# Optimization experiments

Hardware: AMD Instinct MI355X
Metric: run time of the kernel (lower is better)

The kernel has to match this reference:

```python
import jax, jax.numpy as jnp
import numpy as np

BITS = 8
MAX_DELTA = 2.5
QMAX = 2 ** (BITS - 1) - 1  # 127
EPS = 1e-5
K = 3  # kernel size


def _quantize(w):
    # symmetric uniform quantization to `BITS` bits, clamped at +/- MAX_DELTA
    scale = MAX_DELTA / QMAX
    return jnp.clip(jnp.round(w / scale), -QMAX, QMAX) * scale


def _adder_conv(x, wq):
    # AdderNet 'convolution': out[n,co,h,w] = -sum_{ci,kh,kw} |x_patch - wq|
    # x: [N, Cin, H, W]; wq: [Cout, Cin, K, K]; stride 1, padding 1 (same size)
    N, Cin, H, W = x.shape
    Cout = wq.shape[0]
    xp = jnp.pad(x, ((0, 0), (0, 0), (1, 1), (1, 1)))
    out = jnp.zeros((N, Cout, H, W), x.dtype)
    for kh in range(K):            # fixed small loop over kernel taps
        for kw in range(K):
            xs = xp[:, :, kh:kh + H, kw:kw + W]      # [N,Cin,H,W]
            wk = wq[:, :, kh, kw]                    # [Cout,Cin]
            # broadcast [N,1,Cin,H,W] - [1,Cout,Cin,1,1], reduce Cin
            out = out - jnp.sum(jnp.abs(xs[:, None] - wk[None, :, :, None, None]), axis=2)
    return out


def _bn_adder(x, gamma, beta, wb):
    # BatchNorm2d (training-mode batch stats) with the adder weight-bias
    # (per-channel mean |quantized weight|) synced into the affine bias.
    mu = jnp.mean(x, axis=(0, 2, 3), keepdims=True)
    var = jnp.var(x, axis=(0, 2, 3), keepdims=True)
    c = lambda v: v.reshape(1, -1, 1, 1)
    return c(gamma) * (x - mu) * jax.lax.rsqrt(var + EPS) + c(beta) + c(wb)


def setup_inputs() -> dict:
    key = jax.random.key(0)
    k = jax.random.split(key, 3)
    N, C, H, W = 32, 32, 32, 32
    x = jax.random.normal(k[0], (N, C, H, W), jnp.float32)
    w1 = jax.random.normal(k[1], (C, C, K, K), jnp.float32) * 0.1
    w2 = jax.random.normal(k[2], (C, C, K, K), jnp.float32) * 0.1
    return {
        "x": x,
        "w1": w1, "gamma1": jnp.ones(C, jnp.float32), "beta1": jnp.zeros(C, jnp.float32),
        "w2": w2, "gamma2": jnp.ones(C, jnp.float32), "beta2": jnp.zeros(C, jnp.float32),
    }


def reference(x, w1, gamma1, beta1, w2, gamma2, beta2):
    residual = x
    wq1 = _quantize(w1)
    out = _adder_conv(x, wq1)
    wb1 = jnp.mean(jnp.abs(wq1), axis=(1, 2, 3))   # adder weight bias, per out-channel
    out = _bn_adder(out, gamma1, beta1, wb1)
    out = jax.nn.relu(out)
    wq2 = _quantize(w2)
    out = _adder_conv(out, wq2)
    wb2 = jnp.mean(jnp.abs(wq2), axis=(1, 2, 3))
    out = _bn_adder(out, gamma2, beta2, wb2)
    out = jax.nn.relu(out + residual)
    return out
```

## Files before the change

kernel.cpp:

```cpp
#include <hip/hip_runtime.h>


#define QSCALE (2.5f / 127.f)

__device__ __forceinline__ float quantf(float w) {
  float v = rintf(w * (1.0f / QSCALE));
  v = fminf(fmaxf(v, -127.f), 127.f);
  return v * QSCALE;
}

__global__ __launch_bounds__(256) void quant_k(const float* __restrict__ w1,
                                               const float* __restrict__ w2,
                                               float* __restrict__ q1,
                                               float* __restrict__ q2) {
  int i = blockIdx.x * 256 + threadIdx.x;
  if (i >= 18432) return;
  const float* w = (i < 9216) ? w1 : w2;
  float* dst = (i < 9216) ? q1 : q2;
  int j = (i < 9216) ? i : i - 9216;
  int co = j / 288;
  int r = j - co * 288;
  dst[r * 32 + co] = quantf(w[j]);
}

template <bool AFFINE>
__global__ __launch_bounds__(1024, 4) void conv_k(
    const float* __restrict__ in,
    const float* __restrict__ wq,
    const float* __restrict__ ps_prev,
    const float* __restrict__ pq_prev,
    const float* __restrict__ wq_prev,
    const float* __restrict__ gprev,
    const float* __restrict__ bprev,
    float* __restrict__ outb,
    float* __restrict__ ps_out,
    float* __restrict__ pq_out) {
  __shared__ __align__(16) float smem[16128];
  __shared__ float r2a[32][32], r2b[32][32], r2c[32][32];
  __shared__ float abuf[32], bbuf[32];

  float* xs = smem;
  float* wls = smem + 6912;

  const int tid = threadIdx.x;
  const int blk = blockIdx.x;
  const int n = blk >> 3, rg = blk & 7;
  const int h0 = rg << 2;

  if (AFFINE) {
    const int c = tid & 31, ch = tid >> 5;
    float s = 0.f, q = 0.f;
    #pragma unroll
    for (int k = 0; k < 8; ++k) {
      s += ps_prev[(ch * 8 + k) * 32 + c];
      q += pq_prev[(ch * 8 + k) * 32 + c];
    }
    float wbp = 0.f;
    #pragma unroll
    for (int uu = 0; uu < 9; ++uu)
      wbp += fabsf(wq_prev[(ch * 9 + uu) * 32 + c]);
    r2a[c][ch] = s; r2b[c][ch] = q; r2c[c][ch] = wbp;
    __syncthreads();
    if (tid < 32) {
      double S = 0.0, Q = 0.0; float W = 0.f;
      #pragma unroll 8
      for (int k = 0; k < 32; ++k) {
        S += (double)r2a[tid][k]; Q += (double)r2b[tid][k]; W += r2c[tid][k];
      }
      const double M = 32768.0;
      const double mu = S / M;
      const double var = Q / M - mu * mu;
      const double inv = 1.0 / sqrt(var + 1e-5);
      const double g = (double)gprev[tid];
      abuf[tid] = (float)(g * inv);
      bbuf[tid] = (float)((double)bprev[tid] + (double)(W * (1.f / 288.f)) - g * inv * mu);
    }
    __syncthreads();
  }

  {
    const float4* src = (const float4*)wq;
    float4* dst = (float4*)wls;
    for (int i = tid; i < 2304; i += 1024) dst[i] = src[i];
  }
  for (int i = tid; i < 1728; i += 1024) {
    const int ci = i / 54;
    const int rem = i - ci * 54;
    const int tr = rem / 9, k = rem - tr * 9;
    const int h = h0 - 1 + tr;
    float* dst = xs + ci * 216 + tr * 36;
    if (k < 8) {
      float4 v = {0.f, 0.f, 0.f, 0.f};
      if ((unsigned)h < 32u) {
        v = *(const float4*)(in + (((n * 32 + ci) * 32 + h) * 32 + 4 * k));
        if (AFFINE) {
          const float av = abuf[ci], bv = bbuf[ci];
          v.x = fmaxf(fmaf(av, v.x, bv), 0.f);
          v.y = fmaxf(fmaf(av, v.y, bv), 0.f);
          v.z = fmaxf(fmaf(av, v.z, bv), 0.f);
          v.w = fmaxf(fmaf(av, v.w, bv), 0.f);
        }
      }
      dst[4 * k + 1] = v.x; dst[4 * k + 2] = v.y;
      dst[4 * k + 3] = v.z; dst[4 * k + 4] = v.w;
    } else {
      dst[0] = 0.f; dst[33] = 0.f; dst[34] = 0.f; dst[35] = 0.f;
    }
  }
  __syncthreads();

  const int wv = tid >> 6;
  const int oct = wv & 3, slice = wv >> 2;
  const int l = tid & 63;
  const int quad = l >> 5, p = l & 31;
  const int row = p >> 3, g = p & 7;

  float acc[4][4];
  #pragma unroll
  for (int j = 0; j < 4; ++j)
    #pragma unroll
    for (int k = 0; k < 4; ++k) acc[j][k] = 0.f;

  const float* xpb = xs + row * 36 + 4 * g;
  const float* wpb = wls + oct * 8 + quad * 4;

  #pragma unroll 2
  for (int cc = 0; cc < 8; ++cc) {
    const int ci = slice * 8 + cc;
    const float* xp = xpb + ci * 216;
    float xw[3][6];
    #pragma unroll
    for (int kh = 0; kh < 3; ++kh) {
      const float4 A = *(const float4*)(xp + kh * 36);
      const float2 B = *(const float2*)(xp + kh * 36 + 4);
      xw[kh][0] = A.x; xw[kh][1] = A.y; xw[kh][2] = A.z; xw[kh][3] = A.w;
      xw[kh][4] = B.x; xw[kh][5] = B.y;
    }
    const float* wp = wpb + ci * 288;
    #pragma unroll
    for (int t = 0; t < 9; ++t) {
      const float4 W = *(const float4*)(wp + t * 32);
      const int kh = t / 3, kw = t - kh * 3;
      #pragma unroll
      for (int j = 0; j < 4; ++j) {
        const float xv = xw[kh][j + kw];
        acc[j][0] += fabsf(xv - W.x);
        acc[j][1] += fabsf(xv - W.y);
        acc[j][2] += fabsf(xv - W.z);
        acc[j][3] += fabsf(xv - W.w);
      }
    }
  }
  __syncthreads();

  float* red = smem;
  const int lane16 = oct * 64 + l;
  if (slice != 0) {
    const int sb = (slice - 1) * 16;
    #pragma unroll
    for (int j = 0; j < 4; ++j)
      #pragma unroll
      for (int k = 0; k < 4; ++k)
        red[(sb + j * 4 + k) * 256 + lane16] = acc[j][k];
  }
  __syncthreads();

  if (slice == 0) {
    #pragma unroll
    for (int s = 0; s < 3; ++s)
      #pragma unroll
      for (int j = 0; j < 4; ++j)
        #pragma unroll
        for (int k = 0; k < 4; ++k)
          acc[j][k] += red[(s * 16 + j * 4 + k) * 256 + lane16];

    const int h = h0 + row;
    float sv[4], qv[4];
    #pragma unroll
    for (int k = 0; k < 4; ++k) {
      const int co = oct * 8 + quad * 4 + k;
      float4 st;
      st.x = -acc[0][k]; st.y = -acc[1][k]; st.z = -acc[2][k]; st.w = -acc[3][k];
      *(float4*)&outb[((n * 32 + co) * 32 + h) * 32 + 4 * g] = st;
      sv[k] = st.x + st.y + st.z + st.w;
      qv[k] = st.x*st.x + st.y*st.y + st.z*st.z + st.w*st.w;
    }
    #pragma unroll
    for (int d = 1; d < 32; d <<= 1) {
      #pragma unroll
      for (int k = 0; k < 4; ++k) {
        sv[k] += __shfl_xor(sv[k], d);
        qv[k] += __shfl_xor(qv[k], d);
      }
    }
    if (p == 0) {
      const int chunk = n * 8 + rg;
      float4 s4; s4.x = sv[0]; s4.y = sv[1]; s4.z = sv[2]; s4.w = sv[3];
      float4 q4; q4.x = qv[0]; q4.y = qv[1]; q4.z = qv[2]; q4.w = qv[3];
      ((float4*)(ps_out + chunk * 32))[oct * 2 + quad] = s4;
      ((float4*)(pq_out + chunk * 32))[oct * 2 + quad] = q4;
    }
  }
}

__global__ __launch_bounds__(512) void final_k(
    const float* __restrict__ o2, const float* __restrict__ xres,
    const float* __restrict__ ps, const float* __restrict__ pq,
    const float* __restrict__ wq2, const float* __restrict__ g2,
    const float* __restrict__ b2, float* __restrict__ out) {
  __shared__ float r2a[32][16], r2b[32][16], r2c[32][16];
  __shared__ float abuf[32], bbuf[32];
  const int tid = threadIdx.x;
  const int c = tid & 31, ch = tid >> 5;
  float s = 0.f, q = 0.f;
  #pragma unroll
  for (int k = 0; k < 16; ++k) {
    s += ps[(ch * 16 + k) * 32 + c];
    q += pq[(ch * 16 + k) * 32 + c];
  }
  float wbp = 0.f;
  #pragma unroll
  for (int uu = 0; uu < 18; ++uu)
    wbp += fabsf(wq2[(ch * 18 + uu) * 32 + c]);
  r2a[c][ch] = s; r2b[c][ch] = q; r2c[c][ch] = wbp;
  __syncthreads();
  if (tid < 32) {
    double S = 0.0, Q = 0.0; float W = 0.f;
    #pragma unroll
    for (int k = 0; k < 16; ++k) {
      S += (double)r2a[tid][k]; Q += (double)r2b[tid][k]; W += r2c[tid][k];
    }
    const double M = 32768.0;
    const double mu = S / M;
    const double var = Q / M - mu * mu;
    const double inv = 1.0 / sqrt(var + 1e-5);
    const double g = (double)g2[tid];
    abuf[tid] = (float)(g * inv);
    bbuf[tid] = (float)((double)b2[tid] + (double)(W * (1.f / 288.f)) - g * inv * mu);
  }
  __syncthreads();

  const int f4 = blockIdx.x * 512 + tid;
  const int cc = (f4 >> 8) & 31;
  const float4 o = ((const float4*)o2)[f4];
  const float4 xr = ((const float4*)xres)[f4];
  const float av = abuf[cc], bvv = bbuf[cc];
  float4 r;
  r.x = fmaxf(fmaf(av, o.x, bvv) + xr.x, 0.f);
  r.y = fmaxf(fmaf(av, o.y, bvv) + xr.y, 0.f);
  r.z = fmaxf(fmaf(av, o.z, bvv) + xr.z, 0.f);
  r.w = fmaxf(fmaf(av, o.w, bvv) + xr.w, 0.f);
  ((float4*)out)[f4] = r;
}

extern "C" void kernel_launch(void* const* d_in, const int* in_sizes, int n_in,
                              void* d_out, int out_size, void* d_ws, size_t ws_size,
                              hipStream_t stream) {
  const float* x   = (const float*)d_in[0];
  const float* w1  = (const float*)d_in[1];
  const float* g1  = (const float*)d_in[2];
  const float* be1 = (const float*)d_in[3];
  const float* w2  = (const float*)d_in[4];
  const float* g2  = (const float*)d_in[5];
  const float* be2 = (const float*)d_in[6];
  float* ws = (float*)d_ws;

  float* WQ1 = ws;
  float* WQ2 = ws + 9216;
  float* PS1 = ws + 18432;
  float* PQ1 = ws + 26624;
  float* PS2 = ws + 34816;
  float* PQ2 = ws + 43008;
  float* O1  = ws + 51200;
  float* O2  = O1 + 1048576;
  float* out = (float*)d_out;

  quant_k<<<72, 256, 0, stream>>>(w1, w2, WQ1, WQ2);
  conv_k<false><<<256, 1024, 0, stream>>>(x, WQ1, nullptr, nullptr, nullptr,
                                          nullptr, nullptr, O1, PS1, PQ1);
  conv_k<true><<<256, 1024, 0, stream>>>(O1, WQ2, PS1, PQ1, WQ1, g1, be1,
                                         O2, PS2, PQ2);
  final_k<<<512, 512, 0, stream>>>(O2, x, PS2, PQ2, WQ2, g2, be2, out);
}
```

Before: 60.06 us.

## Split conv input channels across two blocks and add merge kernel for stats

Each conv kernel now processes half of the input channels per block, doubling the grid to 512 blocks and cutting shared memory per block. Partial outputs go to separate buffers, and a new merge kernel sums the halves and computes per-sample, per-channel sum and sum-of-squares for batch norm. The intent is more parallelism and occupancy in the conv stage. In exchange it adds two kernel launches and extra global memory round trips for the partial outputs.

```diff
diff --git a/kernel.cpp b/kernel.cpp
--- a/kernel.cpp
+++ b/kernel.cpp
@@ -32,40 +32,40 @@
     const float* __restrict__ wq_prev,
     const float* __restrict__ gprev,
     const float* __restrict__ bprev,
-    float* __restrict__ outb,
-    float* __restrict__ ps_out,
-    float* __restrict__ pq_out) {
-  __shared__ __align__(16) float smem[16128];
-  __shared__ float r2a[32][32], r2b[32][32], r2c[32][32];
+    float* __restrict__ outb) {
+  __shared__ __align__(16) float smem[12288];
   __shared__ float abuf[32], bbuf[32];
 
   float* xs = smem;
-  float* wls = smem + 6912;
+  float* wls = smem + 3456;
 
   const int tid = threadIdx.x;
   const int blk = blockIdx.x;
-  const int n = blk >> 3, rg = blk & 7;
+  const int n = blk >> 4;
+  const int rg = (blk >> 1) & 7;
+  const int cih = blk & 1;
   const int h0 = rg << 2;
 
   if (AFFINE) {
+    float* r2a = smem;
+    float* r2b = smem + 1024;
+    float* r2c = smem + 2048;
     const int c = tid & 31, ch = tid >> 5;
-    float s = 0.f, q = 0.f;
-    #pragma unroll
-    for (int k = 0; k < 8; ++k) {
-      s += ps_prev[(ch * 8 + k) * 32 + c];
-      q += pq_prev[(ch * 8 + k) * 32 + c];
-    }
+    const float s = ps_prev[ch * 32 + c];
+    const float q = pq_prev[ch * 32 + c];
     float wbp = 0.f;
     #pragma unroll
     for (int uu = 0; uu < 9; ++uu)
       wbp += fabsf(wq_prev[(ch * 9 + uu) * 32 + c]);
-    r2a[c][ch] = s; r2b[c][ch] = q; r2c[c][ch] = wbp;
+    r2a[c * 32 + ch] = s; r2b[c * 32 + ch] = q; r2c[c * 32 + ch] = wbp;
     __syncthreads();
     if (tid < 32) {
       double S = 0.0, Q = 0.0; float W = 0.f;
       #pragma unroll 8
       for (int k = 0; k < 32; ++k) {
-        S += (double)r2a[tid][k]; Q += (double)r2b[tid][k]; W += r2c[tid][k];
+        S += (double)r2a[tid * 32 + k];
+        Q += (double)r2b[tid * 32 + k];
+        W += r2c[tid * 32 + k];
       }
       const double M = 32768.0;
       const double mu = S / M;
@@ -81,14 +81,15 @@
   {
     const float4* src = (const float4*)wq;
     float4* dst = (float4*)wls;
-    for (int i = tid; i < 2304; i += 1024) dst[i] = src[i];
-  }
-  for (int i = tid; i < 1728; i += 1024) {
-    const int ci = i / 54;
-    const int rem = i - ci * 54;
+    for (int i = tid; i < 1152; i += 1024) dst[i] = src[cih * 1152 + i];
+  }
+  if (tid < 864) {
+    const int lci = tid / 54;
+    const int rem = tid - lci * 54;
     const int tr = rem / 9, k = rem - tr * 9;
+    const int ci = cih * 16 + lci;
     const int h = h0 - 1 + tr;
-    float* dst = xs + ci * 216 + tr * 36;
+    float* dst = xs + lci * 216 + tr * 36;
     if (k < 8) {
       float4 v = {0.f, 0.f, 0.f, 0.f};
       if ((unsigned)h < 32u) {
@@ -123,11 +124,12 @@
 
   const float* xpb = xs + row * 36 + 4 * g;
   const float* wpb = wls + oct * 8 + quad * 4;
+  const int lci0 = slice * 4;
 
   #pragma unroll 2
-  for (int cc = 0; cc < 8; ++cc) {
-    const int ci = slice * 8 + cc;
-    const float* xp = xpb + ci * 216;
+  for (int cc = 0; cc < 4; ++cc) {
+    const int lci = lci0 + cc;
+    const float* xp = xpb + lci * 216;
     float xw[3][6];
     #pragma unroll
     for (int kh = 0; kh < 3; ++kh) {
@@ -136,7 +138,7 @@
       xw[kh][0] = A.x; xw[kh][1] = A.y; xw[kh][2] = A.z; xw[kh][3] = A.w;
       xw[kh][4] = B.x; xw[kh][5] = B.y;
     }
-    const float* wp = wpb + ci * 288;
+    const float* wp = wpb + lci * 288;
     #pragma unroll
     for (int t = 0; t < 9; ++t) {
       const float4 W = *(const float4*)(wp + t * 32);
@@ -174,32 +176,44 @@
         for (int k = 0; k < 4; ++k)
           acc[j][k] += red[(s * 16 + j * 4 + k) * 256 + lane16];
 
+    float* OUT = outb + cih * 1048576;
     const int h = h0 + row;
-    float sv[4], qv[4];
     #pragma unroll
     for (int k = 0; k < 4; ++k) {
       const int co = oct * 8 + quad * 4 + k;
       float4 st;
       st.x = -acc[0][k]; st.y = -acc[1][k]; st.z = -acc[2][k]; st.w = -acc[3][k];
-      *(float4*)&outb[((n * 32 + co) * 32 + h) * 32 + 4 * g] = st;
-      sv[k] = st.x + st.y + st.z + st.w;
-      qv[k] = st.x*st.x + st.y*st.y + st.z*st.z + st.w*st.w;
-    }
-    #pragma unroll
-    for (int d = 1; d < 32; d <<= 1) {
-      #pragma unroll
-      for (int k = 0; k < 4; ++k) {
-        sv[k] += __shfl_xor(sv[k], d);
-        qv[k] += __shfl_xor(qv[k], d);
-      }
-    }
-    if (p == 0) {
-      const int chunk = n * 8 + rg;
-      float4 s4; s4.x = sv[0]; s4.y = sv[1]; s4.z = sv[2]; s4.w = sv[3];
-      float4 q4; q4.x = qv[0]; q4.y = qv[1]; q4.z = qv[2]; q4.w = qv[3];
-      ((float4*)(ps_out + chunk * 32))[oct * 2 + quad] = s4;
-      ((float4*)(pq_out + chunk * 32))[oct * 2 + quad] = q4;
-    }
+      *(float4*)&OUT[((n * 32 + co) * 32 + h) * 32 + 4 * g] = st;
+    }
+  }
+}
+
+__global__ __launch_bounds__(512) void merge_k(
+    float* __restrict__ A, const float* __restrict__ B,
+    float* __restrict__ ps, float* __restrict__ pq) {
+  __shared__ float pss[8], pqq[8];
+  const int tid = threadIdx.x;
+  const int b = blockIdx.x;
+  const int f4 = b * 512 + tid;
+  const float4 a = ((const float4*)A)[f4];
+  const float4 bb = ((const float4*)B)[f4];
+  float4 v;
+  v.x = a.x + bb.x; v.y = a.y + bb.y; v.z = a.z + bb.z; v.w = a.w + bb.w;
+  ((float4*)A)[f4] = v;
+  float s = v.x + v.y + v.z + v.w;
+  float q = v.x*v.x + v.y*v.y + v.z*v.z + v.w*v.w;
+  #pragma unroll
+  for (int d = 32; d; d >>= 1) { s += __shfl_xor(s, d); q += __shfl_xor(q, d); }
+  if ((tid & 63) == 0) { pss[tid >> 6] = s; pqq[tid >> 6] = q; }
+  __syncthreads();
+  if ((tid & 255) == 0) {
+    const int grp = tid >> 8;
+    float S = 0.f, Q = 0.f;
+    #pragma unroll
+    for (int w = 0; w < 4; ++w) { S += pss[grp * 4 + w]; Q += pqq[grp * 4 + w]; }
+    const int n = b >> 4, c = (b & 15) * 2 + grp;
+    ps[n * 32 + c] = S;
+    pq[n * 32 + c] = Q;
   }
 }
 
@@ -212,12 +226,8 @@
   __shared__ float abuf[32], bbuf[32];
   const int tid = threadIdx.x;
   const int c = tid & 31, ch = tid >> 5;
-  float s = 0.f, q = 0.f;
-  #pragma unroll
-  for (int k = 0; k < 16; ++k) {
-    s += ps[(ch * 16 + k) * 32 + c];
-    q += pq[(ch * 16 + k) * 32 + c];
-  }
+  float s = ps[(2 * ch) * 32 + c] + ps[(2 * ch + 1) * 32 + c];
+  float q = pq[(2 * ch) * 32 + c] + pq[(2 * ch + 1) * 32 + c];
   float wbp = 0.f;
   #pragma unroll
   for (int uu = 0; uu < 18; ++uu)
@@ -268,17 +278,20 @@
   float* WQ1 = ws;
   float* WQ2 = ws + 9216;
   float* PS1 = ws + 18432;
-  float* PQ1 = ws + 26624;
-  float* PS2 = ws + 34816;
-  float* PQ2 = ws + 43008;
-  float* O1  = ws + 51200;
-  float* O2  = O1 + 1048576;
+  float* PQ1 = ws + 19456;
+  float* PS2 = ws + 20480;
+  float* PQ2 = ws + 21504;
+  float* O1a = ws + 22528;
+  float* O1b = O1a + 1048576;
+  float* O2b = O1b + 1048576;
   float* out = (float*)d_out;
 
   quant_k<<<72, 256, 0, stream>>>(w1, w2, WQ1, WQ2);
-  conv_k<false><<<256, 1024, 0, stream>>>(x, WQ1, nullptr, nullptr, nullptr,
-                                          nullptr, nullptr, O1, PS1, PQ1);
-  conv_k<true><<<256, 1024, 0, stream>>>(O1, WQ2, PS1, PQ1, WQ1, g1, be1,
-                                         O2, PS2, PQ2);
-  final_k<<<512, 512, 0, stream>>>(O2, x, PS2, PQ2, WQ2, g2, be2, out);
-}
+  conv_k<false><<<512, 1024, 0, stream>>>(x, WQ1, nullptr, nullptr, nullptr,
+                                          nullptr, nullptr, O1a);
+  merge_k<<<512, 512, 0, stream>>>(O1a, O1b, PS1, PQ1);
+  conv_k<true><<<512, 1024, 0, stream>>>(O1a, WQ2, PS1, PQ1, WQ1, g1, be1,
+                                         O1b);
+  merge_k<<<512, 512, 0, stream>>>(O1b, O2b, PS2, PQ2);
+  final_k<<<512, 512, 0, stream>>>(O1b, x, PS2, PQ2, WQ2, g2, be2, out);
+}
```

Result: slower. 76.13 us (+26.7%).
